# Optimization experiments

Measured on AMD Instinct MI355X. Metric: run time of the kernel, lower is better.

## Reference

```python
import jax, jax.numpy as jnp
import numpy as np

EPS = 1e-5

def _act_quant(x):
    # per-token int8 absmax quantization with straight-through estimator
    scale = 127.0 / jnp.clip(jnp.max(jnp.abs(x), axis=-1, keepdims=True), EPS, None)
    q = jnp.clip(jnp.round(x * scale), -128.0, 127.0) / scale
    return x + jax.lax.stop_gradient(q - x)

def _weight_quant(w):
    # per-tensor ternary (1.58-bit) quantization with STE
    scale = 1.0 / jnp.clip(jnp.mean(jnp.abs(w)), EPS, None)
    q = jnp.clip(jnp.round(w * scale), -1.0, 1.0) / scale
    return w + jax.lax.stop_gradient(q - w)

def _bitlinear(x, w, b):
    y = jnp.einsum('bsd,od->bso', _act_quant(x), _weight_quant(w))
    return y + b

def setup_inputs() -> dict:
    key = jax.random.key(0)
    k1, k2, k3, k4, k5 = jax.random.split(key, 5)
    B, S, D, F = 8, 4096, 1024, 3072
    return {
        'x': jax.random.normal(k1, (B, S, D), dtype=jnp.float32),
        'up_w': jax.random.normal(k2, (F, D), dtype=jnp.float32) * 0.125,
        'up_b': jax.random.normal(k3, (F,), dtype=jnp.float32) * 0.01,
        'down_w': jax.random.normal(k4, (D, F), dtype=jnp.float32) * 0.125,
        'down_b': jax.random.normal(k5, (D,), dtype=jnp.float32) * 0.01,
    }

def reference(x, up_w, up_b, down_w, down_b):
    hidden = _bitlinear(x, up_w, up_b)          # [B,S,3072]
    hidden = jnp.square(jax.nn.relu(hidden))    # relu(h)^2
    return _bitlinear(hidden, down_w, down_b)   # [B,S,1024]
```

## Files before the change

### kernel.cpp

```cpp
#include <hip/hip_runtime.h>
#include <hip/hip_bf16.h>
#include <stdint.h>

#define EPS 1e-5f

typedef int v4i __attribute__((ext_vector_type(4)));
typedef const __attribute__((address_space(1))) void g_void;
typedef __attribute__((address_space(3))) void l_void;

__device__ inline float block_max_nw(float v, int nw) {
    __shared__ float s[8];
#pragma unroll
    for (int o = 32; o; o >>= 1) v = fmaxf(v, __shfl_xor(v, o, 64));
    if ((threadIdx.x & 63) == 0) s[threadIdx.x >> 6] = v;
    __syncthreads();
    float m = s[0];
    for (int i = 1; i < nw; ++i) m = fmaxf(m, s[i]);
    return m;
}

__device__ inline float block_sum64x4(float v) {
    __shared__ float s[4];
#pragma unroll
    for (int o = 32; o; o >>= 1) v += __shfl_xor(v, o, 64);
    if ((threadIdx.x & 63) == 0) s[threadIdx.x >> 6] = v;
    __syncthreads();
    return s[0] + s[1] + s[2] + s[3];
}

__global__ __launch_bounds__(256) void abs_sum_part_k(const float4* __restrict__ w,
                                                      int n4, float* __restrict__ part) {
    float s = 0.0f;
    for (int i = blockIdx.x * 256 + threadIdx.x; i < n4; i += 1024 * 256) {
        float4 v = w[i];
        s += fabsf(v.x) + fabsf(v.y) + fabsf(v.z) + fabsf(v.w);
    }
    s = block_sum64x4(s);
    if (threadIdx.x == 0) part[blockIdx.x] = s;
}

__global__ __launch_bounds__(256) void abs_sum_final_k(const float* __restrict__ parts,
                                                       float* __restrict__ sums) {
    const float* p = parts + blockIdx.x * 1024;
    const int t = threadIdx.x;
    float s = p[t] + p[t + 256] + p[t + 512] + p[t + 768];
    s = block_sum64x4(s);
    if (t == 0) sums[blockIdx.x] = s;
}

__global__ __launch_bounds__(256) void wquant_k(const float4* __restrict__ w,
                                                char4* __restrict__ q,
                                                const float* __restrict__ sum) {
    const float mean = fmaxf(sum[0] * (1.0f / 3145728.0f), EPS);
    const float scale = 1.0f / mean;
    const int i = blockIdx.x * 256 + threadIdx.x;
    float4 v = w[i];
    char4 c;
    c.x = (signed char)(int)fmaxf(fminf(rintf(v.x * scale), 1.0f), -1.0f);
    c.y = (signed char)(int)fmaxf(fminf(rintf(v.y * scale), 1.0f), -1.0f);
    c.z = (signed char)(int)fmaxf(fminf(rintf(v.z * scale), 1.0f), -1.0f);
    c.w = (signed char)(int)fmaxf(fminf(rintf(v.w * scale), 1.0f), -1.0f);
    q[i] = c;
}

__global__ __launch_bounds__(256) void aquant_k(const float4* __restrict__ x,
                                                char4* __restrict__ q,
                                                float* __restrict__ deq) {
    const int row = blockIdx.x, t = threadIdx.x;
    const float4 v = x[(size_t)row * 256 + t];
    float m = fmaxf(fmaxf(fabsf(v.x), fabsf(v.y)), fmaxf(fabsf(v.z), fabsf(v.w)));
    m = block_max_nw(m, 4);
    const float mc = fmaxf(m, EPS);
    const float sc = 127.0f / mc;
    char4 c;
    c.x = (signed char)(int)fmaxf(fminf(rintf(v.x * sc), 127.0f), -128.0f);
    c.y = (signed char)(int)fmaxf(fminf(rintf(v.y * sc), 127.0f), -128.0f);
    c.z = (signed char)(int)fmaxf(fminf(rintf(v.z * sc), 127.0f), -128.0f);
    c.w = (signed char)(int)fmaxf(fminf(rintf(v.w * sc), 127.0f), -128.0f);
    q[(size_t)row * 256 + t] = c;
    if (t == 0) deq[row] = mc / 127.0f;
}

__global__ __launch_bounds__(384) void hquant_k(unsigned short* __restrict__ hid,
                                                float* __restrict__ deq) {
    const size_t row = blockIdx.x;
    const int t = threadIdx.x;
    unsigned short* rp = hid + row * 3072;
    const uint4 u = ((const uint4*)rp)[t];
    float v[8];
    {
        uint32_t uu[4] = {u.x, u.y, u.z, u.w};
#pragma unroll
        for (int i = 0; i < 4; ++i) {
            uint32_t lo = uu[i] << 16, hi = uu[i] & 0xFFFF0000u;
            v[2 * i]     = __uint_as_float(lo);
            v[2 * i + 1] = __uint_as_float(hi);
        }
    }
    float m = 0.0f;
#pragma unroll
    for (int i = 0; i < 8; ++i) m = fmaxf(m, fabsf(v[i]));
    m = block_max_nw(m, 6);
    const float mc = fmaxf(m, EPS);
    const float sc = 127.0f / mc;
    uint32_t p0 = 0, p1 = 0;
#pragma unroll
    for (int i = 0; i < 4; ++i) {
        int c = (int)fminf(rintf(v[i] * sc), 127.0f);
        p0 |= (uint32_t)(c & 255) << (8 * i);
    }
#pragma unroll
    for (int i = 0; i < 4; ++i) {
        int c = (int)fminf(rintf(v[4 + i] * sc), 127.0f);
        p1 |= (uint32_t)(c & 255) << (8 * i);
    }
    uint2 pk; pk.x = p0; pk.y = p1;
    ((uint2*)rp)[t] = pk;
    if (t == 0) deq[row] = mc / 127.0f;
}

template <bool RELU2, typename OutT>
__global__ __launch_bounds__(256) void gemm_i8(
    const int8_t* __restrict__ A, int lda,
    const int8_t* __restrict__ B, int ldb,
    OutT* __restrict__ O, int ldo,
    const float* __restrict__ rowDeq,
    const float* __restrict__ sumPtr,
    const float* __restrict__ bias,
    int K, int nTiles) {
    __shared__ __align__(16) char As[128 * 128];
    __shared__ __align__(16) char Bs[128 * 128];
    const int t = threadIdx.x;
    const int lane = t & 63;
    const int w = t >> 6;
    const int xcd = blockIdx.x & 7;
    const int s = blockIdx.x >> 3;
    const int bm = xcd + 8 * (s / nTiles);
    const int bn = s % nTiles;
    const long m0 = (long)bm * 128;
    const long n0 = (long)bn * 128;

    v4i acc[4][4];
#pragma unroll
    for (int i = 0; i < 4; ++i)
#pragma unroll
        for (int j = 0; j < 4; ++j) acc[i][j] = (v4i){0, 0, 0, 0};

    const int mloc = (w >> 1) * 64;
    const int nloc = (w & 1) * 64;
    const int lr = lane & 15;
    const int q4 = lane >> 4;
    const int swz = lr & 7;
    const int srow = lane >> 3;
    const int scol = ((lane & 7) ^ srow) * 16;

    for (int k0 = 0; k0 < K; k0 += 128) {
#pragma unroll
        for (int j = 0; j < 4; ++j) {
            const int rb = (w * 4 + j) * 8;
            const int8_t* ga = A + (m0 + rb + srow) * (long)lda + k0 + scol;
            const int8_t* gb = B + (n0 + rb + srow) * (long)ldb + k0 + scol;
            __builtin_amdgcn_global_load_lds((g_void*)ga,
                                             (l_void*)(As + (w * 4 + j) * 1024), 16, 0, 0);
            __builtin_amdgcn_global_load_lds((g_void*)gb,
                                             (l_void*)(Bs + (w * 4 + j) * 1024), 16, 0, 0);
        }
        __syncthreads();
        v4i af[2][4], bf[2][4];
#pragma unroll
        for (int h = 0; h < 2; ++h) {
            const int p = ((h * 4 + q4) ^ swz) * 16;
#pragma unroll
            for (int i = 0; i < 4; ++i)
                af[h][i] = *(const v4i*)(As + (mloc + i * 16 + lr) * 128 + p);
#pragma unroll
            for (int j = 0; j < 4; ++j)
                bf[h][j] = *(const v4i*)(Bs + (nloc + j * 16 + lr) * 128 + p);
        }
#pragma unroll
        for (int h = 0; h < 2; ++h)
#pragma unroll
            for (int i = 0; i < 4; ++i)
#pragma unroll
                for (int j = 0; j < 4; ++j)
                    acc[i][j] = __builtin_amdgcn_mfma_i32_16x16x64_i8(af[h][i], bf[h][j],
                                                                      acc[i][j], 0, 0, 0);
        __syncthreads();
    }

    const float wdeq = fmaxf(sumPtr[0] * (1.0f / 3145728.0f), EPS);
#pragma unroll
    for (int i = 0; i < 4; ++i) {
#pragma unroll
        for (int r = 0; r < 4; ++r) {
            const long row = m0 + mloc + i * 16 + q4 * 4 + r;
            const float rs = rowDeq[row] * wdeq;
#pragma unroll
            for (int j = 0; j < 4; ++j) {
                const long col = n0 + nloc + j * 16 + lr;
                float val = (float)acc[i][j][r] * rs + bias[col];
                if (RELU2) {
                    val = fmaxf(val, 0.0f);
                    val = val * val;
                }
                O[row * (long)ldo + col] = (OutT)val;
            }
        }
    }
}

extern "C" void kernel_launch(void* const* d_in, const int* in_sizes, int n_in,
                              void* d_out, int out_size, void* d_ws, size_t ws_size,
                              hipStream_t stream) {
    const float* x      = (const float*)d_in[0];
    const float* up_w   = (const float*)d_in[1];
    const float* up_b   = (const float*)d_in[2];
    const float* down_w = (const float*)d_in[3];
    const float* down_b = (const float*)d_in[4];

    char* ws = (char*)d_ws;
    float*  sums   = (float*)ws;
    float*  parts  = (float*)(ws + 256);
    int8_t* qw_dn  = (int8_t*)(ws + 256 + 8192);
    float*  deqh   = (float*)(ws + 256 + 8192 + 3145728);
    __hip_bfloat16* hidden = (__hip_bfloat16*)(ws + 256 + 8192 + 3145728 + 131072);

    int8_t* qx    = (int8_t*)d_out;
    int8_t* qw_up = qx + 33554432;
    float*  deqx  = (float*)(qx + 33554432 + 3145728);

    abs_sum_part_k<<<1024, 256, 0, stream>>>((const float4*)up_w, 786432, parts);
    abs_sum_part_k<<<1024, 256, 0, stream>>>((const float4*)down_w, 786432, parts + 1024);
    abs_sum_final_k<<<2, 256, 0, stream>>>(parts, sums);

    wquant_k<<<3072, 256, 0, stream>>>((const float4*)up_w, (char4*)qw_up, &sums[0]);
    wquant_k<<<3072, 256, 0, stream>>>((const float4*)down_w, (char4*)qw_dn, &sums[1]);
    aquant_k<<<32768, 256, 0, stream>>>((const float4*)x, (char4*)qx, deqx);

    gemm_i8<true, __hip_bfloat16><<<256 * 24, 256, 0, stream>>>(
        qx, 1024, qw_up, 1024, hidden, 3072, deqx, &sums[0], up_b, 1024, 24);
    hquant_k<<<32768, 384, 0, stream>>>((unsigned short*)hidden, deqh);
    gemm_i8<false, float><<<256 * 8, 256, 0, stream>>>(
        (const int8_t*)hidden, 6144, qw_dn, 3072, (float*)d_out, 1024,
        deqh, &sums[1], down_b, 3072, 8);
}
```

Baseline: 569.2 us.

## Widen int8 GEMM tile to 128x256 and switch to 32x32x32 MFMA

The int8 GEMM now uses a 128x256 output tile per block, with each wave computing 64x128 through 32x32x32 i8 MFMAs instead of 16x16x64, and the grid sizes are halved to match. This raises arithmetic intensity per LDS/global byte and cuts LDS fragment reads per MFMA, reducing load overhead in the GEMM main loop. It grows LDS to 48KB and accumulator registers; launch_bounds(256,2) asks for two blocks per CU, which may force register spills or limit occupancy. The loop is still single-buffered with no overlap between loads and compute.

Measured after the change: 527.7 us. -7.3%, faster.

```diff
diff --git a/kernel.cpp b/kernel.cpp
--- a/kernel.cpp
+++ b/kernel.cpp
@@ -5,6 +5,7 @@
 #define EPS 1e-5f
 
 typedef int v4i __attribute__((ext_vector_type(4)));
+typedef int v16i __attribute__((ext_vector_type(16)));
 typedef const __attribute__((address_space(1))) void g_void;
 typedef __attribute__((address_space(3))) void l_void;
 
@@ -120,7 +121,7 @@
 }
 
 template <bool RELU2, typename OutT>
-__global__ __launch_bounds__(256) void gemm_i8(
+__global__ __launch_bounds__(256, 2) void gemm_i8(
     const int8_t* __restrict__ A, int lda,
     const int8_t* __restrict__ B, int ldb,
     OutT* __restrict__ O, int ldo,
@@ -129,7 +130,7 @@
     const float* __restrict__ bias,
     int K, int nTiles) {
     __shared__ __align__(16) char As[128 * 128];
-    __shared__ __align__(16) char Bs[128 * 128];
+    __shared__ __align__(16) char Bs[256 * 128];
     const int t = threadIdx.x;
     const int lane = t & 63;
     const int w = t >> 6;
@@ -138,72 +139,77 @@
     const int bm = xcd + 8 * (s / nTiles);
     const int bn = s % nTiles;
     const long m0 = (long)bm * 128;
-    const long n0 = (long)bn * 128;
-
-    v4i acc[4][4];
-#pragma unroll
-    for (int i = 0; i < 4; ++i)
-#pragma unroll
-        for (int j = 0; j < 4; ++j) acc[i][j] = (v4i){0, 0, 0, 0};
+    const long n0 = (long)bn * 256;
+
+    v16i acc[2][4];
+#pragma unroll
+    for (int i = 0; i < 2; ++i)
+#pragma unroll
+        for (int j = 0; j < 4; ++j) acc[i][j] = (v16i)(0);
 
     const int mloc = (w >> 1) * 64;
-    const int nloc = (w & 1) * 64;
-    const int lr = lane & 15;
-    const int q4 = lane >> 4;
-    const int swz = lr & 7;
+    const int nloc = (w & 1) * 128;
+    const int r32 = lane & 31;
+    const int h = lane >> 5;
+    const int swz = r32 & 7;
     const int srow = lane >> 3;
     const int scol = ((lane & 7) ^ srow) * 16;
 
+    const int8_t* pa = A + (m0 + w * 8 + srow) * (long)lda + scol;
+    const int8_t* pb = B + (n0 + w * 8 + srow) * (long)ldb + scol;
+
+    int cs[4];
+#pragma unroll
+    for (int ks = 0; ks < 4; ++ks) cs[ks] = ((ks * 2 + h) ^ swz) * 16;
+
     for (int k0 = 0; k0 < K; k0 += 128) {
 #pragma unroll
-        for (int j = 0; j < 4; ++j) {
-            const int rb = (w * 4 + j) * 8;
-            const int8_t* ga = A + (m0 + rb + srow) * (long)lda + k0 + scol;
-            const int8_t* gb = B + (n0 + rb + srow) * (long)ldb + k0 + scol;
-            __builtin_amdgcn_global_load_lds((g_void*)ga,
-                                             (l_void*)(As + (w * 4 + j) * 1024), 16, 0, 0);
-            __builtin_amdgcn_global_load_lds((g_void*)gb,
-                                             (l_void*)(Bs + (w * 4 + j) * 1024), 16, 0, 0);
+        for (int r = 0; r < 4; ++r)
+            __builtin_amdgcn_global_load_lds((g_void*)(pa + (long)r * 32 * lda + k0),
+                                             (l_void*)(As + r * 4096 + w * 1024), 16, 0, 0);
+#pragma unroll
+        for (int r = 0; r < 8; ++r)
+            __builtin_amdgcn_global_load_lds((g_void*)(pb + (long)r * 32 * ldb + k0),
+                                             (l_void*)(Bs + r * 4096 + w * 1024), 16, 0, 0);
+        __syncthreads();
+#pragma unroll
+        for (int ks = 0; ks < 4; ++ks) {
+            v4i af[2], bf[4];
+#pragma unroll
+            for (int mt = 0; mt < 2; ++mt)
+                af[mt] = *(const v4i*)(As + (mloc + mt * 32 + r32) * 128 + cs[ks]);
+#pragma unroll
+            for (int nt = 0; nt < 4; ++nt)
+                bf[nt] = *(const v4i*)(Bs + (nloc + nt * 32 + r32) * 128 + cs[ks]);
+#pragma unroll
+            for (int mt = 0; mt < 2; ++mt)
+#pragma unroll
+                for (int nt = 0; nt < 4; ++nt)
+                    acc[mt][nt] = __builtin_amdgcn_mfma_i32_32x32x32_i8(
+                        af[mt], bf[nt], acc[mt][nt], 0, 0, 0);
         }
         __syncthreads();
-        v4i af[2][4], bf[2][4];
-#pragma unroll
-        for (int h = 0; h < 2; ++h) {
-            const int p = ((h * 4 + q4) ^ swz) * 16;
-#pragma unroll
-            for (int i = 0; i < 4; ++i)
-                af[h][i] = *(const v4i*)(As + (mloc + i * 16 + lr) * 128 + p);
-#pragma unroll
-            for (int j = 0; j < 4; ++j)
-                bf[h][j] = *(const v4i*)(Bs + (nloc + j * 16 + lr) * 128 + p);
-        }
-#pragma unroll
-        for (int h = 0; h < 2; ++h)
-#pragma unroll
-            for (int i = 0; i < 4; ++i)
-#pragma unroll
-                for (int j = 0; j < 4; ++j)
-                    acc[i][j] = __builtin_amdgcn_mfma_i32_16x16x64_i8(af[h][i], bf[h][j],
-                                                                      acc[i][j], 0, 0, 0);
-        __syncthreads();
     }
 
     const float wdeq = fmaxf(sumPtr[0] * (1.0f / 3145728.0f), EPS);
 #pragma unroll
-    for (int i = 0; i < 4; ++i) {
-#pragma unroll
-        for (int r = 0; r < 4; ++r) {
-            const long row = m0 + mloc + i * 16 + q4 * 4 + r;
-            const float rs = rowDeq[row] * wdeq;
-#pragma unroll
-            for (int j = 0; j < 4; ++j) {
-                const long col = n0 + nloc + j * 16 + lr;
-                float val = (float)acc[i][j][r] * rs + bias[col];
-                if (RELU2) {
-                    val = fmaxf(val, 0.0f);
-                    val = val * val;
+    for (int mt = 0; mt < 2; ++mt) {
+#pragma unroll
+        for (int g = 0; g < 4; ++g) {
+#pragma unroll
+            for (int rr = 0; rr < 4; ++rr) {
+                const long row = m0 + mloc + mt * 32 + g * 8 + h * 4 + rr;
+                const float rs = rowDeq[row] * wdeq;
+#pragma unroll
+                for (int nt = 0; nt < 4; ++nt) {
+                    const long col = n0 + nloc + nt * 32 + r32;
+                    float val = (float)acc[mt][nt][g * 4 + rr] * rs + bias[col];
+                    if (RELU2) {
+                        val = fmaxf(val, 0.0f);
+                        val = val * val;
+                    }
+                    O[row * (long)ldo + col] = (OutT)val;
                 }
-                O[row * (long)ldo + col] = (OutT)val;
             }
         }
     }
@@ -237,10 +243,10 @@
     wquant_k<<<3072, 256, 0, stream>>>((const float4*)down_w, (char4*)qw_dn, &sums[1]);
     aquant_k<<<32768, 256, 0, stream>>>((const float4*)x, (char4*)qx, deqx);
 
-    gemm_i8<true, __hip_bfloat16><<<256 * 24, 256, 0, stream>>>(
-        qx, 1024, qw_up, 1024, hidden, 3072, deqx, &sums[0], up_b, 1024, 24);
+    gemm_i8<true, __hip_bfloat16><<<3072, 256, 0, stream>>>(
+        qx, 1024, qw_up, 1024, hidden, 3072, deqx, &sums[0], up_b, 1024, 12);
     hquant_k<<<32768, 384, 0, stream>>>((unsigned short*)hidden, deqh);
-    gemm_i8<false, float><<<256 * 8, 256, 0, stream>>>(
+    gemm_i8<false, float><<<1024, 256, 0, stream>>>(
         (const int8_t*)hidden, 6144, qw_dn, 3072, (float*)d_out, 1024,
-        deqh, &sums[1], down_b, 3072, 8);
-}
+        deqh, &sums[1], down_b, 3072, 4);
+}
```
